# Kernel optimization log

Measured on AMD Instinct MI355X. Metric: run time of the kernel, lower is better.

The kernel has to match this reference:

```python
import jax, jax.numpy as jnp
import numpy as np

N = 50000            # num_node
E = 800000           # num edges (avg degree 16)
DIN = [128, 128, 64, 64, 32]   # nfeat, 4h, 2h, 2h, h
DOUT = [128, 64, 64, 32, 16]   # 4h, 2h, 2h, h, nclass
KAPPA = 0.9
N_FP_ITERS = 15      # fixed-point solver iterations (fixed count, jit-friendly)
N_POWER_ITERS = 50   # power iteration for spectral radius


def setup_inputs() -> dict:
    key = jax.random.key(0)
    ks = jax.random.split(key, 4 + 4 * 5)
    inp = {}
    inp["features"] = jax.random.normal(ks[0], (DIN[0], N), dtype=jnp.float32)
    inp["row"] = jax.random.randint(ks[1], (E,), 0, N, dtype=jnp.int32)
    inp["col"] = jax.random.randint(ks[2], (E,), 0, N, dtype=jnp.int32)
    inp["val"] = jax.random.uniform(ks[3], (E,), dtype=jnp.float32) * 0.1
    for i in range(5):
        din, dout = DIN[i], DOUT[i]
        inp[f"W{i}"] = jax.random.normal(ks[4 + 4 * i], (dout, dout), dtype=jnp.float32) * 0.05
        inp[f"Om{i}"] = jax.random.normal(ks[5 + 4 * i], (dout, din), dtype=jnp.float32) * (1.0 / np.sqrt(din))
        inp[f"Pw{i}"] = jax.random.normal(ks[6 + 4 * i], (dout, din), dtype=jnp.float32) * (1.0 / np.sqrt(din))
        inp[f"Pb{i}"] = jnp.zeros((dout,), dtype=jnp.float32)
    return inp


def spmm_AT(row, col, val, X):
    # A^T @ X for node-major X: [N, m]; A[row[e], col[e]] = val[e]
    return jax.ops.segment_sum(X[row] * val[:, None], col, num_segments=N)


def spmv_A(row, col, val, v):
    # (A v)[i] = sum_j A[i, j] v[j]
    return jax.ops.segment_sum(val * v[col], row, num_segments=N)


def spectral_rad(row, col, val):
    # power iteration (replaces scipy sparse eigs in get_spectral_rad)
    def step(v, _):
        w = spmv_A(row, col, val, v)
        return w / (jnp.linalg.norm(w) + 1e-12), None
    v0 = jnp.full((N,), 1.0 / np.sqrt(N), dtype=val.dtype)
    v, _ = jax.lax.scan(step, v0, None, length=N_POWER_ITERS)
    return jnp.linalg.norm(spmv_A(row, col, val, v)) + 1e-12


def project_inf_norm(W, k):
    # project each row of W onto the L1 ball of radius k (=> ||W||_inf <= k)
    a = jnp.abs(W)
    s = jnp.sort(a, axis=1)[:, ::-1]                 # descending
    cs = jnp.cumsum(s, axis=1)
    idx = jnp.arange(1, W.shape[1] + 1, dtype=W.dtype)
    nnz = jnp.sum(s - (cs - k) / idx > 0, axis=1)    # support size, >= 1
    cs_at = jnp.take_along_axis(cs, (nnz - 1)[:, None], axis=1)[:, 0]
    theta = jnp.maximum((cs_at - k) / nnz.astype(W.dtype), 0.0)
    Wp = jnp.sign(W) * jnp.maximum(a - theta[:, None], 0.0)
    return jnp.where((jnp.sum(a, axis=1) > k)[:, None], Wp, W)


def ignn_layer(row, col, val, rho, W, Om, Xt):
    # fixed point of Z = relu(W Z A + Om X A); node-major: Zt = relu(A^T Zt W^T + bt)
    Wp = project_inf_norm(W, KAPPA / rho)
    bt = spmm_AT(row, col, val, Xt @ Om.T)           # [N, dout]
    @jax.checkpoint
    def step(Z, _):
        return jax.nn.relu(spmm_AT(row, col, val, Z) @ Wp.T + bt), None
    Z, _ = jax.lax.scan(step, jnp.zeros_like(bt), None, length=N_FP_ITERS)
    return Z


def _forward(features, row, col, val, Ws, Oms, Pws, Pbs):
    rho = jax.lax.stop_gradient(spectral_rad(row, col, val))
    x = features.T                                   # node-major [N, din]
    for i in range(5):
        z = ignn_layer(row, col, val, rho, Ws[i], Oms[i], x)
        x = z + x @ Pws[i].T + Pbs[i]                # z_star + proj(x)
        if i < 4:
            x = jax.nn.elu(x)
    return x                                         # [N, nclass] (== x.T in the torch code)


def reference(features, row, col, val,
              W0, W1, W2, W3, W4,
              Om0, Om1, Om2, Om3, Om4,
              Pw0, Pw1, Pw2, Pw3, Pw4,
              Pb0, Pb1, Pb2, Pb3, Pb4):
    Ws = [W0, W1, W2, W3, W4]
    Oms = [Om0, Om1, Om2, Om3, Om4]
    Pws = [Pw0, Pw1, Pw2, Pw3, Pw4]
    Pbs = [Pb0, Pb1, Pb2, Pb3, Pb4]
    return _forward(features, row, col, val, Ws, Oms, Pws, Pbs)
```

## Files before the change

### kernel.cpp

```cpp
#include <hip/hip_runtime.h>
#include <hip/hip_fp16.h>
#include <math.h>

#define THREADS 256

static inline int ceil_div(int a, int b) { return (a + b - 1) / b; }

__device__ __forceinline__ float wave_sum_all(float v) {
#pragma unroll
  for (int m = 1; m < 64; m <<= 1) v += __shfl_xor(v, m);
  return v;
}
__device__ __forceinline__ float wave_max_all(float v) {
#pragma unroll
  for (int m = 1; m < 64; m <<= 1) v = fmaxf(v, __shfl_xor(v, m));
  return v;
}

template <int D>
__device__ __forceinline__ float2 gather_row2h(const int* __restrict__ crow,
                                               const float* __restrict__ cval,
                                               const __half* __restrict__ Z, int e0, int e1,
                                               int jj2) {
  float2 acc[8];
#pragma unroll
  for (int u = 0; u < 8; ++u) acc[u] = make_float2(0.f, 0.f);
  for (int e = e0; e < e1; e += 8) {
    int r[8];
    float v[8];
#pragma unroll
    for (int u = 0; u < 8; ++u) {
      int ee = e + u;
      bool ok = ee < e1;
      r[u] = ok ? crow[ee] : 0;
      v[u] = ok ? cval[ee] : 0.f;
    }
    __half2 z[8];
#pragma unroll
    for (int u = 0; u < 8; ++u) z[u] = *(const __half2*)&Z[(size_t)r[u] * D + jj2];
#pragma unroll
    for (int u = 0; u < 8; ++u) {
      float2 f = __half22float2(z[u]);
      acc[u].x += v[u] * f.x;
      acc[u].y += v[u] * f.y;
    }
  }
  float2 s01 = make_float2(acc[0].x + acc[1].x, acc[0].y + acc[1].y);
  float2 s23 = make_float2(acc[2].x + acc[3].x, acc[2].y + acc[3].y);
  float2 s45 = make_float2(acc[4].x + acc[5].x, acc[4].y + acc[5].y);
  float2 s67 = make_float2(acc[6].x + acc[7].x, acc[6].y + acc[7].y);
  return make_float2((s01.x + s23.x) + (s45.x + s67.x), (s01.y + s23.y) + (s45.y + s67.y));
}


__global__ __launch_bounds__(THREADS) void zero_i32(int* p, int n) {
  int i = blockIdx.x * THREADS + threadIdx.x;
  if (i < n) p[i] = 0;
}

__global__ __launch_bounds__(THREADS) void init_power(float* v, float* norm2, int n, float c) {
  int i = blockIdx.x * THREADS + threadIdx.x;
  if (i < n) v[i] = c;
  if (blockIdx.x == 0 && threadIdx.x < 64) norm2[threadIdx.x] = 0.f;
}

__global__ __launch_bounds__(THREADS) void hist_deg(const int* __restrict__ row,
                                                    const int* __restrict__ col,
                                                    int* rdeg, int* cdeg, int E) {
  int e = blockIdx.x * THREADS + threadIdx.x;
  if (e < E) {
    atomicAdd(&rdeg[row[e]], 1);
    atomicAdd(&cdeg[col[e]], 1);
  }
}

__global__ __launch_bounds__(THREADS) void scan1(const int* __restrict__ in, int* bsum, int L) {
  __shared__ int lds[THREADS];
  int idx = blockIdx.x * THREADS + threadIdx.x;
  lds[threadIdx.x] = (idx < L) ? in[idx] : 0;
  __syncthreads();
  for (int off = THREADS / 2; off > 0; off >>= 1) {
    if (threadIdx.x < off) lds[threadIdx.x] += lds[threadIdx.x + off];
    __syncthreads();
  }
  if (threadIdx.x == 0) bsum[blockIdx.x] = lds[0];
}

__global__ __launch_bounds__(THREADS) void scan2(int* bsum, int B) {
  __shared__ int lds[THREADS];
  int t = threadIdx.x;
  lds[t] = (t < B) ? bsum[t] : 0;
  __syncthreads();
  for (int off = 1; off < THREADS; off <<= 1) {
    int add = (t >= off) ? lds[t - off] : 0;
    __syncthreads();
    lds[t] += add;
    __syncthreads();
  }
  if (t < B) bsum[t] = (t == 0) ? 0 : lds[t - 1];
}

__global__ __launch_bounds__(THREADS) void scan3(int* data, const int* __restrict__ bsum, int L) {
  __shared__ int lds[THREADS];
  int t = threadIdx.x;
  int idx = blockIdx.x * THREADS + t;
  int v = (idx < L) ? data[idx] : 0;
  lds[t] = v;
  __syncthreads();
  for (int off = 1; off < THREADS; off <<= 1) {
    int add = (t >= off) ? lds[t - off] : 0;
    __syncthreads();
    lds[t] += add;
    __syncthreads();
  }
  if (idx < L) data[idx] = lds[t] - v + bsum[blockIdx.x];
}

__global__ __launch_bounds__(THREADS) void scatter_edges(
    const int* __restrict__ row, const int* __restrict__ col, const float* __restrict__ val,
    const int* __restrict__ rstart, int* rcur, int* csr_col, float* csr_val,
    const int* __restrict__ cstart, int* ccur, int* csc_row, float* csc_val, int E) {
  int e = blockIdx.x * THREADS + threadIdx.x;
  if (e < E) {
    int r = row[e], c = col[e];
    float v = val[e];
    int p = rstart[r] + atomicAdd(&rcur[r], 1);
    csr_col[p] = c;
    csr_val[p] = v;
    int q = cstart[c] + atomicAdd(&ccur[c], 1);
    csc_row[q] = r;
    csc_val[q] = v;
  }
}

__global__ __launch_bounds__(THREADS) void power_spmv_nn(
    const int* __restrict__ rs, const int* __restrict__ rcol, const float* __restrict__ rval,
    const float* __restrict__ vin, float* __restrict__ vout, int n) {
  int gid = blockIdx.x * THREADS + threadIdx.x;
  int node = gid >> 2;
  int sl = gid & 3;
  if (node >= n) return;
  int e0 = rs[node], e1 = rs[node + 1];
  float a0 = 0.f, a1 = 0.f, a2 = 0.f, a3 = 0.f;
  for (int e = e0 + sl; e < e1; e += 16) {
    int ee1 = e + 4, ee2 = e + 8, ee3 = e + 12;
    bool k1 = ee1 < e1, k2 = ee2 < e1, k3 = ee3 < e1;
    int r0 = rcol[e];
    int r1 = k1 ? rcol[ee1] : 0;
    int r2 = k2 ? rcol[ee2] : 0;
    int r3 = k3 ? rcol[ee3] : 0;
    float v0 = rval[e];
    float v1 = k1 ? rval[ee1] : 0.f;
    float v2 = k2 ? rval[ee2] : 0.f;
    float v3 = k3 ? rval[ee3] : 0.f;
    a0 += v0 * vin[r0];
    a1 += v1 * vin[r1];
    a2 += v2 * vin[r2];
    a3 += v3 * vin[r3];
  }
  float w = (a0 + a1) + (a2 + a3);
  w += __shfl_xor(w, 1);
  w += __shfl_xor(w, 2);
  if (sl == 0) vout[node] = w;
}

__global__ __launch_bounds__(THREADS) void norm2_pair(const float* __restrict__ u,
                                                      const float* __restrict__ w,
                                                      float* norm2, int n) {
  int i = blockIdx.x * THREADS + threadIdx.x;
  float a = (i < n) ? u[i] : 0.f;
  float b = (i < n) ? w[i] : 0.f;
  float sa = wave_sum_all(a * a);
  float sb = wave_sum_all(b * b);
  __shared__ float pa[4], pb[4];
  if ((threadIdx.x & 63) == 0) {
    pa[threadIdx.x >> 6] = sa;
    pb[threadIdx.x >> 6] = sb;
  }
  __syncthreads();
  if (threadIdx.x == 0) atomicAdd(&norm2[0], pa[0] + pa[1] + pa[2] + pa[3]);
  if (threadIdx.x == 64) atomicAdd(&norm2[1], pb[0] + pb[1] + pb[2] + pb[3]);
}


__global__ __launch_bounds__(256) void transpose_feat(const float* __restrict__ in,
                                                      float* __restrict__ out, int n) {
  __shared__ float tile[32][33];
  int bx = blockIdx.x;
  int by = blockIdx.y;
  int x = bx * 32 + threadIdx.x;
  for (int dy = threadIdx.y; dy < 32; dy += 8) {
    int y = by * 32 + dy;
    tile[dy][threadIdx.x] = (x < n) ? in[(size_t)y * n + x] : 0.f;
  }
  __syncthreads();
  for (int dy = threadIdx.y; dy < 32; dy += 8) {
    int node = bx * 32 + dy;
    int feat = by * 32 + threadIdx.x;
    if (node < n) out[(size_t)node * 128 + feat] = tile[threadIdx.x][dy];
  }
}

__global__ __launch_bounds__(THREADS) void transpose_small(const float* __restrict__ in,
                                                           float* __restrict__ out, int rows,
                                                           int cols) {
  int idx = blockIdx.x * THREADS + threadIdx.x;
  if (idx < rows * cols) {
    int r = idx / cols, c = idx % cols;
    out[c * rows + r] = in[idx];
  }
}

template <int D>
__global__ __launch_bounds__(64) void project_row(const float* __restrict__ W,
                                                  float* __restrict__ WpT,
                                                  const float* __restrict__ norm2) {
  int o = blockIdx.x;
  int l = threadIdx.x;
  float rho = sqrtf(norm2[0] / norm2[1]) + 1e-12f;
  float k = 0.9f / rho;
  float a0 = (l < D) ? W[o * D + l] : 0.f;
  float a1 = (64 + l < D) ? W[o * D + 64 + l] : 0.f;
  float ab0 = fabsf(a0), ab1 = fabsf(a1);
  float s = wave_sum_all(ab0 + ab1);
  float mx = wave_max_all(fmaxf(ab0, ab1));
  float w0 = a0, w1 = a1;
  if (s > k) {
    float lo = 0.f, hi = mx;
    for (int it = 0; it < 50; ++it) {
      float mid = 0.5f * (lo + hi);
      float g = wave_sum_all(fmaxf(ab0 - mid, 0.f) + fmaxf(ab1 - mid, 0.f));
      if (g > k) lo = mid; else hi = mid;
    }
    float theta = 0.5f * (lo + hi);
    w0 = copysignf(fmaxf(ab0 - theta, 0.f), a0);
    w1 = copysignf(fmaxf(ab1 - theta, 0.f), a1);
  }
  if (l < D) WpT[l * D + o] = w0;
  if (64 + l < D) WpT[(64 + l) * D + o] = w1;
}

template <int DOUT>
__global__ __launch_bounds__(THREADS, 8) void spmm_bt(
    const int* __restrict__ cstart, const int* __restrict__ crow, const float* __restrict__ cval,
    const __half* __restrict__ X, __half* __restrict__ bt, __half* __restrict__ Zinit, int n) {
  constexpr int HD = DOUT / 2;
  int idx = blockIdx.x * THREADS + threadIdx.x;
  int node = idx / HD;
  int jj2 = (idx % HD) * 2;
  if (node >= n) return;
  int e0 = cstart[node], e1 = cstart[node + 1];
  float2 acc = gather_row2h<DOUT>(crow, cval, X, e0, e1, jj2);
  size_t o = (size_t)node * DOUT + jj2;
  *(__half2*)&bt[o] = __floats2half2_rn(acc.x, acc.y);
  *(__half2*)&Zinit[o] = __floats2half2_rn(fmaxf(acc.x, 0.f), fmaxf(acc.y, 0.f));
}

template <int DOUT, int NB>
__global__ __launch_bounds__(THREADS, 8) void fp_step(
    const int* __restrict__ cstart, const int* __restrict__ crow, const float* __restrict__ cval,
    const __half* __restrict__ Zin, const float* __restrict__ WpT, const __half* __restrict__ bt,
    __half* __restrict__ Zout, int n) {
  constexpr int TO = DOUT / 4;
  constexpr int TN = THREADS / TO;
  constexpr int NT = NB / TN;
  static_assert(NT >= 1, "NB too small");
  __shared__ float sT[NB][DOUT + 2];
  const int node0 = blockIdx.x * NB;
  const int tid = threadIdx.x;
  {
    constexpr int HD = DOUT / 2;
    constexpr int LG = THREADS / HD;
    const int jj2 = (tid % HD) * 2;
    const int lg = tid / HD;
    for (int nn = lg; nn < NB; nn += LG) {
      int node = node0 + nn;
      float2 acc = make_float2(0.f, 0.f);
      if (node < n) {
        int e0 = cstart[node], e1 = cstart[node + 1];
        acc = gather_row2h<DOUT>(crow, cval, Zin, e0, e1, jj2);
      }
      *(float2*)&sT[nn][jj2] = acc;
    }
  }
  __syncthreads();
  const int o4 = tid % TO, tg = tid / TO;
  const int o0 = o4 * 4;
  float acc[NT][4];
#pragma unroll
  for (int a = 0; a < NT; ++a) acc[a][0] = acc[a][1] = acc[a][2] = acc[a][3] = 0.f;
  for (int jz = 0; jz < DOUT; ++jz) {
    const float4 w4 = *(const float4*)&WpT[jz * DOUT + o0];
#pragma unroll
    for (int a = 0; a < NT; ++a) {
      float sv = sT[tg * NT + a][jz];
      acc[a][0] += sv * w4.x;
      acc[a][1] += sv * w4.y;
      acc[a][2] += sv * w4.z;
      acc[a][3] += sv * w4.w;
    }
  }
#pragma unroll
  for (int a = 0; a < NT; ++a) {
    int node = node0 + tg * NT + a;
    if (node < n) {
      size_t o = (size_t)node * DOUT + o0;
      float2 b01 = __half22float2(*(const __half2*)&bt[o]);
      float2 b23 = __half22float2(*(const __half2*)&bt[o + 2]);
      float zx = fmaxf(acc[a][0] + b01.x, 0.f);
      float zy = fmaxf(acc[a][1] + b01.y, 0.f);
      float zz = fmaxf(acc[a][2] + b23.x, 0.f);
      float zw = fmaxf(acc[a][3] + b23.y, 0.f);
      *(__half2*)&Zout[o] = __floats2half2_rn(zx, zy);
      *(__half2*)&Zout[o + 2] = __floats2half2_rn(zz, zw);
    }
  }
}

template <int DOUT, int NB, bool OUTH>
__global__ __launch_bounds__(THREADS) void dense_gemm(
    const float* __restrict__ X, int din, const float* __restrict__ MT,
    const float* __restrict__ bias, const __half* __restrict__ Addh, int act,
    void* __restrict__ OutV, int n) {
  constexpr int TO = DOUT / 4;
  constexpr int TN = THREADS / TO;
  constexpr int NT = NB / TN;
  __shared__ float xs[NB][129];
  const int node0 = blockIdx.x * NB;
  const int tid = threadIdx.x;
  for (int idx = tid; idx < NB * din; idx += THREADS) {
    int nn = idx / din, j = idx % din;
    int node = node0 + nn;
    xs[nn][j] = (node < n) ? X[(size_t)node * din + j] : 0.f;
  }
  __syncthreads();
  const int o4 = tid % TO, tg = tid / TO;
  const int o0 = o4 * 4;
  float acc[NT][4];
#pragma unroll
  for (int a = 0; a < NT; ++a) acc[a][0] = acc[a][1] = acc[a][2] = acc[a][3] = 0.f;
  for (int j = 0; j < din; ++j) {
    const float4 m4 = *(const float4*)&MT[j * DOUT + o0];
#pragma unroll
    for (int a = 0; a < NT; ++a) {
      float sv = xs[tg * NT + a][j];
      acc[a][0] += sv * m4.x;
      acc[a][1] += sv * m4.y;
      acc[a][2] += sv * m4.z;
      acc[a][3] += sv * m4.w;
    }
  }
#pragma unroll
  for (int a = 0; a < NT; ++a) {
    int node = node0 + tg * NT + a;
    if (node < n) {
      float4 r;
      r.x = acc[a][0]; r.y = acc[a][1]; r.z = acc[a][2]; r.w = acc[a][3];
      if (bias) {
        r.x += bias[o0]; r.y += bias[o0 + 1]; r.z += bias[o0 + 2]; r.w += bias[o0 + 3];
      }
      if (Addh) {
        size_t o = (size_t)node * DOUT + o0;
        float2 a01 = __half22float2(*(const __half2*)&Addh[o]);
        float2 a23 = __half22float2(*(const __half2*)&Addh[o + 2]);
        r.x += a01.x; r.y += a01.y; r.z += a23.x; r.w += a23.y;
      }
      if (act == 1) {
        r.x = (r.x > 0.f) ? r.x : expm1f(r.x);
        r.y = (r.y > 0.f) ? r.y : expm1f(r.y);
        r.z = (r.z > 0.f) ? r.z : expm1f(r.z);
        r.w = (r.w > 0.f) ? r.w : expm1f(r.w);
      }
      size_t o = (size_t)node * DOUT + o0;
      if (OUTH) {
        __half* O = (__half*)OutV;
        *(__half2*)&O[o] = __floats2half2_rn(r.x, r.y);
        *(__half2*)&O[o + 2] = __floats2half2_rn(r.z, r.w);
      } else {
        float* O = (float*)OutV;
        *(float4*)&O[o] = r;
      }
    }
  }
}


static void launch_project(int dout, const float* W, float* WpT, const float* norm2,
                           hipStream_t s) {
  switch (dout) {
    case 128: project_row<128><<<128, 64, 0, s>>>(W, WpT, norm2); break;
    case 64: project_row<64><<<64, 64, 0, s>>>(W, WpT, norm2); break;
    case 32: project_row<32><<<32, 64, 0, s>>>(W, WpT, norm2); break;
    case 16: project_row<16><<<16, 64, 0, s>>>(W, WpT, norm2); break;
  }
}

static void launch_spmm_bt(int dout, const int* cs, const int* cr, const float* cv,
                           const __half* X, __half* bt, __half* Zi, int n, hipStream_t s) {
  int g = ceil_div(n * dout / 2, THREADS);
  switch (dout) {
    case 128: spmm_bt<128><<<g, THREADS, 0, s>>>(cs, cr, cv, X, bt, Zi, n); break;
    case 64: spmm_bt<64><<<g, THREADS, 0, s>>>(cs, cr, cv, X, bt, Zi, n); break;
    case 32: spmm_bt<32><<<g, THREADS, 0, s>>>(cs, cr, cv, X, bt, Zi, n); break;
    case 16: spmm_bt<16><<<g, THREADS, 0, s>>>(cs, cr, cv, X, bt, Zi, n); break;
  }
}

static void launch_fp_step(int dout, const int* cs, const int* cr, const float* cv,
                           const __half* Zin, const float* WpT, const __half* bt, __half* Zout,
                           int n, hipStream_t s) {
  switch (dout) {
    case 128: fp_step<128, 16><<<ceil_div(n, 16), THREADS, 0, s>>>(cs, cr, cv, Zin, WpT, bt, Zout, n); break;
    case 64: fp_step<64, 16><<<ceil_div(n, 16), THREADS, 0, s>>>(cs, cr, cv, Zin, WpT, bt, Zout, n); break;
    case 32: fp_step<32, 32><<<ceil_div(n, 32), THREADS, 0, s>>>(cs, cr, cv, Zin, WpT, bt, Zout, n); break;
    case 16: fp_step<16, 64><<<ceil_div(n, 64), THREADS, 0, s>>>(cs, cr, cv, Zin, WpT, bt, Zout, n); break;
  }
}

static void launch_dense_gemm_h(int dout, const float* X, int din, const float* MT,
                                __half* Out, int n, hipStream_t s) {
  switch (dout) {
    case 128: dense_gemm<128, 32, true><<<ceil_div(n, 32), THREADS, 0, s>>>(X, din, MT, nullptr, nullptr, 0, Out, n); break;
    case 64: dense_gemm<64, 32, true><<<ceil_div(n, 32), THREADS, 0, s>>>(X, din, MT, nullptr, nullptr, 0, Out, n); break;
    case 32: dense_gemm<32, 32, true><<<ceil_div(n, 32), THREADS, 0, s>>>(X, din, MT, nullptr, nullptr, 0, Out, n); break;
    case 16: dense_gemm<16, 64, true><<<ceil_div(n, 64), THREADS, 0, s>>>(X, din, MT, nullptr, nullptr, 0, Out, n); break;
  }
}

static void launch_dense_gemm_f(int dout, const float* X, int din, const float* MT,
                                const float* bias, const __half* Addh, int act, float* Out,
                                int n, hipStream_t s) {
  switch (dout) {
    case 128: dense_gemm<128, 32, false><<<ceil_div(n, 32), THREADS, 0, s>>>(X, din, MT, bias, Addh, act, Out, n); break;
    case 64: dense_gemm<64, 32, false><<<ceil_div(n, 32), THREADS, 0, s>>>(X, din, MT, bias, Addh, act, Out, n); break;
    case 32: dense_gemm<32, 32, false><<<ceil_div(n, 32), THREADS, 0, s>>>(X, din, MT, bias, Addh, act, Out, n); break;
    case 16: dense_gemm<16, 64, false><<<ceil_div(n, 64), THREADS, 0, s>>>(X, din, MT, bias, Addh, act, Out, n); break;
  }
}

extern "C" void kernel_launch(void* const* d_in, const int* in_sizes, int n_in, void* d_out,
                              int out_size, void* d_ws, size_t ws_size, hipStream_t stream) {
  const float* features = (const float*)d_in[0];
  const int* row = (const int*)d_in[1];
  const int* col = (const int*)d_in[2];
  const float* val = (const float*)d_in[3];
  const int N = in_sizes[0] / 128;
  const int E = in_sizes[1];
  static const int DIN[5] = {128, 128, 64, 64, 32};
  static const int DOUT[5] = {128, 64, 64, 32, 16};

  char* base = (char*)d_ws;
  size_t off = 0;
  auto alloc = [&](size_t bytes) -> void* {
    off = (off + 255) & ~(size_t)255;
    void* p = (void*)(base + off);
    off += bytes;
    return p;
  };

  int* rstart = (int*)alloc((size_t)(N + 1) * 4);
  int* cstart = (int*)alloc((size_t)(N + 1) * 4);
  int* rcur = (int*)alloc((size_t)N * 4);
  int* ccur = (int*)alloc((size_t)N * 4);
  int* bsum = (int*)alloc(256 * 4);
  float* norm2 = (float*)alloc(64 * 4);
  float* v_a = (float*)alloc((size_t)N * 4);
  float* v_b = (float*)alloc((size_t)N * 4);
  int* csr_col = (int*)alloc((size_t)E * 4);
  float* csr_val = (float*)alloc((size_t)E * 4);
  int* csc_row = (int*)alloc((size_t)E * 4);
  float* csc_val = (float*)alloc((size_t)E * 4);
  float* WpT = (float*)alloc(16384 * 4);
  float* OmT = (float*)alloc(16384 * 4);
  float* PwT = (float*)alloc(16384 * 4);
  float* x0 = (float*)alloc((size_t)N * 128 * 4);
  float* x1 = (float*)alloc((size_t)N * 128 * 4);
  __half* xom = (__half*)alloc((size_t)N * 128 * 2);
  __half* btb = (__half*)alloc((size_t)N * 128 * 2);
  __half* z_a = (__half*)alloc((size_t)N * 128 * 2);
  __half* z_b = (__half*)alloc((size_t)N * 128 * 2);

  const int gN = ceil_div(N, THREADS);
  const int gE = ceil_div(E, THREADS);
  const int L = N + 1;
  const int B = ceil_div(L, THREADS);

  zero_i32<<<ceil_div(N + 1, THREADS), THREADS, 0, stream>>>(rstart, N + 1);
  zero_i32<<<ceil_div(N + 1, THREADS), THREADS, 0, stream>>>(cstart, N + 1);
  zero_i32<<<gN, THREADS, 0, stream>>>(rcur, N);
  zero_i32<<<gN, THREADS, 0, stream>>>(ccur, N);
  init_power<<<gN, THREADS, 0, stream>>>(v_a, norm2, N, (float)(1.0 / sqrt((double)N)));
  hist_deg<<<gE, THREADS, 0, stream>>>(row, col, rstart, cstart, E);
  scan1<<<B, THREADS, 0, stream>>>(rstart, bsum, L);
  scan2<<<1, THREADS, 0, stream>>>(bsum, B);
  scan3<<<B, THREADS, 0, stream>>>(rstart, bsum, L);
  scan1<<<B, THREADS, 0, stream>>>(cstart, bsum, L);
  scan2<<<1, THREADS, 0, stream>>>(bsum, B);
  scan3<<<B, THREADS, 0, stream>>>(cstart, bsum, L);
  scatter_edges<<<gE, THREADS, 0, stream>>>(row, col, val, rstart, rcur, csr_col, csr_val,
                                            cstart, ccur, csc_row, csc_val, E);

  {
    dim3 grid(ceil_div(N, 32), 4);
    dim3 block(32, 8);
    transpose_feat<<<grid, block, 0, stream>>>(features, x0, N);
  }

  {
    int g4 = ceil_div(N * 4, THREADS);
    for (int k = 1; k <= 51; ++k) {
      const float* vin = (k & 1) ? v_a : v_b;
      float* vout = (k & 1) ? v_b : v_a;
      power_spmv_nn<<<g4, THREADS, 0, stream>>>(rstart, csr_col, csr_val, vin, vout, N);
    }
    norm2_pair<<<gN, THREADS, 0, stream>>>(v_b, v_a, norm2, N);
  }

  float* xcur = x0;
  float* xnext = x1;
  for (int i = 0; i < 5; ++i) {
    const int din = DIN[i], dout = DOUT[i];
    const float* W = (const float*)d_in[4 + 4 * i];
    const float* Om = (const float*)d_in[5 + 4 * i];
    const float* Pw = (const float*)d_in[6 + 4 * i];
    const float* Pb = (const float*)d_in[7 + 4 * i];

    transpose_small<<<ceil_div(dout * din, THREADS), THREADS, 0, stream>>>(Om, OmT, dout, din);
    transpose_small<<<ceil_div(dout * din, THREADS), THREADS, 0, stream>>>(Pw, PwT, dout, din);
    launch_project(dout, W, WpT, norm2, stream);

    launch_dense_gemm_h(dout, xcur, din, OmT, xom, N, stream);
    launch_spmm_bt(dout, cstart, csc_row, csc_val, xom, btb, z_a, N, stream);
    for (int s = 0; s < 14; ++s) {
      const __half* zin = (s & 1) ? z_b : z_a;
      __half* zout = (s & 1) ? z_a : z_b;
      launch_fp_step(dout, cstart, csc_row, csc_val, zin, WpT, btb, zout, N, stream);
    }
    float* outp = (i < 4) ? xnext : (float*)d_out;
    launch_dense_gemm_f(dout, xcur, din, PwT, Pb, z_a, (i < 4) ? 1 : 0, outp, N, stream);
    float* t = xcur; xcur = xnext; xnext = t;
  }
}
```

Before: 4.799 ms.

## Pack CSC row/value into int2 and drop CSR build, power-iterate on A^T

Stores each column-sorted edge as an interleaved int2 of (row index, float value bits), so the sparse gathers load index and weight with one 8-byte load instead of two separate loads from two arrays. It also removes the row-major CSR structure entirely: no row histogram, no row scan and no CSR scatter. Power iteration now runs on the CSC arrays, which computes A^T v, relying on A and A^T having the same spectral radius. The risk is that the estimate after a fixed number of iterations can differ slightly from the A-based reference.

```diff
diff --git a/kernel.cpp b/kernel.cpp
--- a/kernel.cpp
+++ b/kernel.cpp
@@ -18,31 +18,28 @@
 }
 
 template <int D>
-__device__ __forceinline__ float2 gather_row2h(const int* __restrict__ crow,
-                                               const float* __restrict__ cval,
+__device__ __forceinline__ float2 gather_row2h(const int2* __restrict__ edges,
                                                const __half* __restrict__ Z, int e0, int e1,
                                                int jj2) {
   float2 acc[8];
 #pragma unroll
   for (int u = 0; u < 8; ++u) acc[u] = make_float2(0.f, 0.f);
   for (int e = e0; e < e1; e += 8) {
-    int r[8];
-    float v[8];
+    int2 ev[8];
 #pragma unroll
     for (int u = 0; u < 8; ++u) {
       int ee = e + u;
-      bool ok = ee < e1;
-      r[u] = ok ? crow[ee] : 0;
-      v[u] = ok ? cval[ee] : 0.f;
+      ev[u] = (ee < e1) ? edges[ee] : make_int2(0, 0);
     }
     __half2 z[8];
 #pragma unroll
-    for (int u = 0; u < 8; ++u) z[u] = *(const __half2*)&Z[(size_t)r[u] * D + jj2];
+    for (int u = 0; u < 8; ++u) z[u] = *(const __half2*)&Z[(size_t)ev[u].x * D + jj2];
 #pragma unroll
     for (int u = 0; u < 8; ++u) {
+      float v = __int_as_float(ev[u].y);
       float2 f = __half22float2(z[u]);
-      acc[u].x += v[u] * f.x;
-      acc[u].y += v[u] * f.y;
+      acc[u].x += v * f.x;
+      acc[u].y += v * f.y;
     }
   }
   float2 s01 = make_float2(acc[0].x + acc[1].x, acc[0].y + acc[1].y);
@@ -64,14 +61,10 @@
   if (blockIdx.x == 0 && threadIdx.x < 64) norm2[threadIdx.x] = 0.f;
 }
 
-__global__ __launch_bounds__(THREADS) void hist_deg(const int* __restrict__ row,
-                                                    const int* __restrict__ col,
-                                                    int* rdeg, int* cdeg, int E) {
+__global__ __launch_bounds__(THREADS) void hist_c(const int* __restrict__ col, int* cdeg,
+                                                  int E) {
   int e = blockIdx.x * THREADS + threadIdx.x;
-  if (e < E) {
-    atomicAdd(&rdeg[row[e]], 1);
-    atomicAdd(&cdeg[col[e]], 1);
-  }
+  if (e < E) atomicAdd(&cdeg[col[e]], 1);
 }
 
 __global__ __launch_bounds__(THREADS) void scan1(const int* __restrict__ in, int* bsum, int L) {
@@ -116,47 +109,36 @@
   if (idx < L) data[idx] = lds[t] - v + bsum[blockIdx.x];
 }
 
-__global__ __launch_bounds__(THREADS) void scatter_edges(
+__global__ __launch_bounds__(THREADS) void scatter_edges_c(
     const int* __restrict__ row, const int* __restrict__ col, const float* __restrict__ val,
-    const int* __restrict__ rstart, int* rcur, int* csr_col, float* csr_val,
-    const int* __restrict__ cstart, int* ccur, int* csc_row, float* csc_val, int E) {
+    const int* __restrict__ cstart, int* ccur, int2* __restrict__ csc, int E) {
   int e = blockIdx.x * THREADS + threadIdx.x;
   if (e < E) {
-    int r = row[e], c = col[e];
-    float v = val[e];
-    int p = rstart[r] + atomicAdd(&rcur[r], 1);
-    csr_col[p] = c;
-    csr_val[p] = v;
+    int c = col[e];
     int q = cstart[c] + atomicAdd(&ccur[c], 1);
-    csc_row[q] = r;
-    csc_val[q] = v;
+    csc[q] = make_int2(row[e], __float_as_int(val[e]));
   }
 }
 
 __global__ __launch_bounds__(THREADS) void power_spmv_nn(
-    const int* __restrict__ rs, const int* __restrict__ rcol, const float* __restrict__ rval,
+    const int* __restrict__ cs, const int2* __restrict__ csc,
     const float* __restrict__ vin, float* __restrict__ vout, int n) {
   int gid = blockIdx.x * THREADS + threadIdx.x;
   int node = gid >> 2;
   int sl = gid & 3;
   if (node >= n) return;
-  int e0 = rs[node], e1 = rs[node + 1];
+  int e0 = cs[node], e1 = cs[node + 1];
   float a0 = 0.f, a1 = 0.f, a2 = 0.f, a3 = 0.f;
   for (int e = e0 + sl; e < e1; e += 16) {
     int ee1 = e + 4, ee2 = e + 8, ee3 = e + 12;
-    bool k1 = ee1 < e1, k2 = ee2 < e1, k3 = ee3 < e1;
-    int r0 = rcol[e];
-    int r1 = k1 ? rcol[ee1] : 0;
-    int r2 = k2 ? rcol[ee2] : 0;
-    int r3 = k3 ? rcol[ee3] : 0;
-    float v0 = rval[e];
-    float v1 = k1 ? rval[ee1] : 0.f;
-    float v2 = k2 ? rval[ee2] : 0.f;
-    float v3 = k3 ? rval[ee3] : 0.f;
-    a0 += v0 * vin[r0];
-    a1 += v1 * vin[r1];
-    a2 += v2 * vin[r2];
-    a3 += v3 * vin[r3];
+    int2 E0 = csc[e];
+    int2 E1 = (ee1 < e1) ? csc[ee1] : make_int2(0, 0);
+    int2 E2 = (ee2 < e1) ? csc[ee2] : make_int2(0, 0);
+    int2 E3 = (ee3 < e1) ? csc[ee3] : make_int2(0, 0);
+    a0 += __int_as_float(E0.y) * vin[E0.x];
+    a1 += __int_as_float(E1.y) * vin[E1.x];
+    a2 += __int_as_float(E2.y) * vin[E2.x];
+    a3 += __int_as_float(E3.y) * vin[E3.x];
   }
   float w = (a0 + a1) + (a2 + a3);
   w += __shfl_xor(w, 1);
@@ -242,7 +224,7 @@
 
 template <int DOUT>
 __global__ __launch_bounds__(THREADS, 8) void spmm_bt(
-    const int* __restrict__ cstart, const int* __restrict__ crow, const float* __restrict__ cval,
+    const int* __restrict__ cstart, const int2* __restrict__ csc,
     const __half* __restrict__ X, __half* __restrict__ bt, __half* __restrict__ Zinit, int n) {
   constexpr int HD = DOUT / 2;
   int idx = blockIdx.x * THREADS + threadIdx.x;
@@ -250,7 +232,7 @@
   int jj2 = (idx % HD) * 2;
   if (node >= n) return;
   int e0 = cstart[node], e1 = cstart[node + 1];
-  float2 acc = gather_row2h<DOUT>(crow, cval, X, e0, e1, jj2);
+  float2 acc = gather_row2h<DOUT>(csc, X, e0, e1, jj2);
   size_t o = (size_t)node * DOUT + jj2;
   *(__half2*)&bt[o] = __floats2half2_rn(acc.x, acc.y);
   *(__half2*)&Zinit[o] = __floats2half2_rn(fmaxf(acc.x, 0.f), fmaxf(acc.y, 0.f));
@@ -258,7 +240,7 @@
 
 template <int DOUT, int NB>
 __global__ __launch_bounds__(THREADS, 8) void fp_step(
-    const int* __restrict__ cstart, const int* __restrict__ crow, const float* __restrict__ cval,
+    const int* __restrict__ cstart, const int2* __restrict__ csc,
     const __half* __restrict__ Zin, const float* __restrict__ WpT, const __half* __restrict__ bt,
     __half* __restrict__ Zout, int n) {
   constexpr int TO = DOUT / 4;
@@ -278,7 +260,7 @@
       float2 acc = make_float2(0.f, 0.f);
       if (node < n) {
         int e0 = cstart[node], e1 = cstart[node + 1];
-        acc = gather_row2h<DOUT>(crow, cval, Zin, e0, e1, jj2);
+        acc = gather_row2h<DOUT>(csc, Zin, e0, e1, jj2);
       }
       *(float2*)&sT[nn][jj2] = acc;
     }
@@ -395,25 +377,25 @@
   }
 }
 
-static void launch_spmm_bt(int dout, const int* cs, const int* cr, const float* cv,
+static void launch_spmm_bt(int dout, const int* cs, const int2* csc,
                            const __half* X, __half* bt, __half* Zi, int n, hipStream_t s) {
   int g = ceil_div(n * dout / 2, THREADS);
   switch (dout) {
-    case 128: spmm_bt<128><<<g, THREADS, 0, s>>>(cs, cr, cv, X, bt, Zi, n); break;
-    case 64: spmm_bt<64><<<g, THREADS, 0, s>>>(cs, cr, cv, X, bt, Zi, n); break;
-    case 32: spmm_bt<32><<<g, THREADS, 0, s>>>(cs, cr, cv, X, bt, Zi, n); break;
-    case 16: spmm_bt<16><<<g, THREADS, 0, s>>>(cs, cr, cv, X, bt, Zi, n); break;
-  }
-}
-
-static void launch_fp_step(int dout, const int* cs, const int* cr, const float* cv,
+    case 128: spmm_bt<128><<<g, THREADS, 0, s>>>(cs, csc, X, bt, Zi, n); break;
+    case 64: spmm_bt<64><<<g, THREADS, 0, s>>>(cs, csc, X, bt, Zi, n); break;
+    case 32: spmm_bt<32><<<g, THREADS, 0, s>>>(cs, csc, X, bt, Zi, n); break;
+    case 16: spmm_bt<16><<<g, THREADS, 0, s>>>(cs, csc, X, bt, Zi, n); break;
+  }
+}
+
+static void launch_fp_step(int dout, const int* cs, const int2* csc,
                            const __half* Zin, const float* WpT, const __half* bt, __half* Zout,
                            int n, hipStream_t s) {
   switch (dout) {
-    case 128: fp_step<128, 16><<<ceil_div(n, 16), THREADS, 0, s>>>(cs, cr, cv, Zin, WpT, bt, Zout, n); break;
-    case 64: fp_step<64, 16><<<ceil_div(n, 16), THREADS, 0, s>>>(cs, cr, cv, Zin, WpT, bt, Zout, n); break;
-    case 32: fp_step<32, 32><<<ceil_div(n, 32), THREADS, 0, s>>>(cs, cr, cv, Zin, WpT, bt, Zout, n); break;
-    case 16: fp_step<16, 64><<<ceil_div(n, 64), THREADS, 0, s>>>(cs, cr, cv, Zin, WpT, bt, Zout, n); break;
+    case 128: fp_step<128, 16><<<ceil_div(n, 16), THREADS, 0, s>>>(cs, csc, Zin, WpT, bt, Zout, n); break;
+    case 64: fp_step<64, 16><<<ceil_div(n, 16), THREADS, 0, s>>>(cs, csc, Zin, WpT, bt, Zout, n); break;
+    case 32: fp_step<32, 32><<<ceil_div(n, 32), THREADS, 0, s>>>(cs, csc, Zin, WpT, bt, Zout, n); break;
+    case 16: fp_step<16, 64><<<ceil_div(n, 64), THREADS, 0, s>>>(cs, csc, Zin, WpT, bt, Zout, n); break;
   }
 }
 
@@ -458,18 +440,14 @@
     return p;
   };
 
-  int* rstart = (int*)alloc((size_t)(N + 1) * 4);
-  int* cstart = (int*)alloc((size_t)(N + 1) * 4);
-  int* rcur = (int*)alloc((size_t)N * 4);
-  int* ccur = (int*)alloc((size_t)N * 4);
+  int* cmeta = (int*)alloc((size_t)(2 * N + 2) * 4);
+  int* cstart = cmeta;
+  int* ccur = cmeta + N + 1;
   int* bsum = (int*)alloc(256 * 4);
   float* norm2 = (float*)alloc(64 * 4);
   float* v_a = (float*)alloc((size_t)N * 4);
   float* v_b = (float*)alloc((size_t)N * 4);
-  int* csr_col = (int*)alloc((size_t)E * 4);
-  float* csr_val = (float*)alloc((size_t)E * 4);
-  int* csc_row = (int*)alloc((size_t)E * 4);
-  float* csc_val = (float*)alloc((size_t)E * 4);
+  int2* csc = (int2*)alloc((size_t)E * 8);
   float* WpT = (float*)alloc(16384 * 4);
   float* OmT = (float*)alloc(16384 * 4);
   float* PwT = (float*)alloc(16384 * 4);
@@ -485,20 +463,13 @@
   const int L = N + 1;
   const int B = ceil_div(L, THREADS);
 
-  zero_i32<<<ceil_div(N + 1, THREADS), THREADS, 0, stream>>>(rstart, N + 1);
-  zero_i32<<<ceil_div(N + 1, THREADS), THREADS, 0, stream>>>(cstart, N + 1);
-  zero_i32<<<gN, THREADS, 0, stream>>>(rcur, N);
-  zero_i32<<<gN, THREADS, 0, stream>>>(ccur, N);
+  zero_i32<<<ceil_div(2 * N + 1, THREADS), THREADS, 0, stream>>>(cmeta, 2 * N + 1);
   init_power<<<gN, THREADS, 0, stream>>>(v_a, norm2, N, (float)(1.0 / sqrt((double)N)));
-  hist_deg<<<gE, THREADS, 0, stream>>>(row, col, rstart, cstart, E);
-  scan1<<<B, THREADS, 0, stream>>>(rstart, bsum, L);
-  scan2<<<1, THREADS, 0, stream>>>(bsum, B);
-  scan3<<<B, THREADS, 0, stream>>>(rstart, bsum, L);
+  hist_c<<<gE, THREADS, 0, stream>>>(col, cstart, E);
   scan1<<<B, THREADS, 0, stream>>>(cstart, bsum, L);
   scan2<<<1, THREADS, 0, stream>>>(bsum, B);
   scan3<<<B, THREADS, 0, stream>>>(cstart, bsum, L);
-  scatter_edges<<<gE, THREADS, 0, stream>>>(row, col, val, rstart, rcur, csr_col, csr_val,
-                                            cstart, ccur, csc_row, csc_val, E);
+  scatter_edges_c<<<gE, THREADS, 0, stream>>>(row, col, val, cstart, ccur, csc, E);
 
   {
     dim3 grid(ceil_div(N, 32), 4);
@@ -511,7 +482,7 @@
     for (int k = 1; k <= 51; ++k) {
       const float* vin = (k & 1) ? v_a : v_b;
       float* vout = (k & 1) ? v_b : v_a;
-      power_spmv_nn<<<g4, THREADS, 0, stream>>>(rstart, csr_col, csr_val, vin, vout, N);
+      power_spmv_nn<<<g4, THREADS, 0, stream>>>(cstart, csc, vin, vout, N);
     }
     norm2_pair<<<gN, THREADS, 0, stream>>>(v_b, v_a, norm2, N);
   }
@@ -530,11 +501,11 @@
     launch_project(dout, W, WpT, norm2, stream);
 
     launch_dense_gemm_h(dout, xcur, din, OmT, xom, N, stream);
-    launch_spmm_bt(dout, cstart, csc_row, csc_val, xom, btb, z_a, N, stream);
+    launch_spmm_bt(dout, cstart, csc, xom, btb, z_a, N, stream);
     for (int s = 0; s < 14; ++s) {
       const __half* zin = (s & 1) ? z_b : z_a;
       __half* zout = (s & 1) ? z_a : z_b;
-      launch_fp_step(dout, cstart, csc_row, csc_val, zin, WpT, btb, zout, N, stream);
+      launch_fp_step(dout, cstart, csc, zin, WpT, btb, zout, N, stream);
     }
     float* outp = (i < 4) ? xnext : (float*)d_out;
     launch_dense_gemm_f(dout, xcur, din, PwT, Pb, z_a, (i < 4) ? 1 : 0, outp, N, stream);
```

Result: no change. 4.844 ms (+0.9%).
